# Performance work log

Hardware: AMD Instinct MI355X
Metric: run time of the kernel (lower is better)

The kernel has to match this reference:

```python
import jax, jax.numpy as jnp
import numpy as np

D = 256; NH = 8; NL = 4; NP = 4; DFF = 1024; BS = 8; NQ = 300
DH = D // NH
EPS = 1e-5
SPATIAL = np.array([[100, 150], [50, 75], [25, 38], [13, 19]], dtype=np.int64)  # (H, W) per level
SIZES = (SPATIAL[:, 0] * SPATIAL[:, 1])
S = int(SIZES.sum())  # 19947
LSI = np.concatenate([[0], np.cumsum(SIZES)[:-1]]).astype(np.int64)


def setup_inputs() -> dict:
    key = jax.random.key(0)
    ks = iter(jax.random.split(key, 48))
    def nrm(shape, s=0.02):
        return jax.random.normal(next(ks), shape, jnp.float32) * s
    return {
        "tgt": jax.random.normal(next(ks), (BS, NQ, D), jnp.float32),
        "tgt_query_pos": jax.random.normal(next(ks), (BS, NQ, D), jnp.float32),
        "tgt_reference_points": jax.random.uniform(next(ks), (BS, NQ, NL, 2), jnp.float32),
        "memory": jax.random.normal(next(ks), (BS, S, D), jnp.float32),
        "memory_key_padding_mask": jnp.zeros((BS, S), jnp.bool_),
        "memory_spatial_shapes": jnp.asarray(SPATIAL),
        "memory_level_start_index": jnp.asarray(LSI),
        # self-attention (nn.MultiheadAttention) params
        "in_proj_w": nrm((3 * D, D)), "in_proj_b": jnp.zeros((3 * D,), jnp.float32),
        "out_proj_w": nrm((D, D)), "out_proj_b": jnp.zeros((D,), jnp.float32),
        # layernorms
        "norm1_g": jnp.ones((D,), jnp.float32), "norm1_b": jnp.zeros((D,), jnp.float32),
        "norm2_g": jnp.ones((D,), jnp.float32), "norm2_b": jnp.zeros((D,), jnp.float32),
        "norm3_g": jnp.ones((D,), jnp.float32), "norm3_b": jnp.zeros((D,), jnp.float32),
        # MSDeformAttn params
        "samp_off_w": nrm((NH * NL * NP * 2, D)), "samp_off_b": nrm((NH * NL * NP * 2,), 0.5),
        "attn_wt_w": nrm((NH * NL * NP, D)), "attn_wt_b": jnp.zeros((NH * NL * NP,), jnp.float32),
        "value_w": nrm((D, D)), "value_b": jnp.zeros((D,), jnp.float32),
        "outp_w": nrm((D, D)), "outp_b": jnp.zeros((D,), jnp.float32),
        # FFN params
        "lin1_w": nrm((DFF, D)), "lin1_b": jnp.zeros((DFF,), jnp.float32),
        "lin2_w": nrm((D, DFF)), "lin2_b": jnp.zeros((D,), jnp.float32),
    }


def _ln(x, g, b):
    m = x.mean(-1, keepdims=True)
    v = ((x - m) ** 2).mean(-1, keepdims=True)
    return (x - m) / jnp.sqrt(v + EPS) * g + b


def _self_attn(tgt, pos, in_w, in_b, ow, ob):
    bs, nq, _ = tgt.shape
    qk = tgt + pos
    qw, kw, vw = jnp.split(in_w, 3, axis=0)
    qb, kb, vb = jnp.split(in_b, 3)
    proj = lambda x, w, b: (x @ w.T + b).reshape(bs, nq, NH, DH)
    qh, kh, vh = proj(qk, qw, qb), proj(qk, kw, kb), proj(tgt, vw, vb)
    logits = jnp.einsum('bqhd,bkhd->bhqk', qh, kh) / np.sqrt(DH).astype(np.float32)
    a = jax.nn.softmax(logits, axis=-1)
    o = jnp.einsum('bhqk,bkhd->bqhd', a, vh).reshape(bs, nq, D)
    return o @ ow.T + ob


def _msdeform(query, ref, memory, pad_mask, so_w, so_b, aw_w, aw_b, vw, vb, ow, ob):
    bs, nq, _ = query.shape
    value = memory @ vw.T + vb
    value = jnp.where(pad_mask[..., None], 0.0, value).reshape(bs, S, NH, DH)
    off = (query @ so_w.T + so_b).reshape(bs, nq, NH, NL, NP, 2)
    aw = jax.nn.softmax((query @ aw_w.T + aw_b).reshape(bs, nq, NH, NL * NP), axis=-1)
    aw = aw.reshape(bs, nq, NH, NL, NP)
    # offset normalizer is (W, H) per level
    normalizer = jnp.asarray(SPATIAL[:, ::-1].copy(), jnp.float32)
    locs = ref[:, :, None, :, None, :] + off / normalizer[None, None, None, :, None, :]
    out = jnp.zeros((bs, nq, NH, DH), jnp.float32)
    for l in range(NL):
        Hl, Wl = int(SPATIAL[l, 0]), int(SPATIAL[l, 1])
        s0 = int(LSI[l])
        v = value[:, s0:s0 + Hl * Wl]  # [bs, Hl*Wl, NH, DH]
        # grid_sample(align_corners=False) pixel mapping
        x = locs[:, :, :, l, :, 0] * Wl - 0.5  # [bs, nq, NH, NP]
        y = locs[:, :, :, l, :, 1] * Hl - 0.5
        x0f, y0f = jnp.floor(x), jnp.floor(y)
        tx, ty = x - x0f, y - y0f
        x0, y0 = x0f.astype(jnp.int32), y0f.astype(jnp.int32)
        samp = jnp.zeros(x.shape + (DH,), jnp.float32)
        for dy, dx, w in ((0, 0, (1 - ty) * (1 - tx)), (0, 1, (1 - ty) * tx),
                          (1, 0, ty * (1 - tx)), (1, 1, ty * tx)):
            xi, yi = x0 + dx, y0 + dy
            valid = (xi >= 0) & (xi < Wl) & (yi >= 0) & (yi < Hl)  # zero padding
            idx = jnp.clip(yi, 0, Hl - 1) * Wl + jnp.clip(xi, 0, Wl - 1)
            idx2 = idx.swapaxes(2, 3).reshape(bs, nq * NP, NH)
            g = jnp.take_along_axis(v, idx2[..., None], axis=1)  # [bs, nq*NP, NH, DH]
            g = g.reshape(bs, nq, NP, NH, DH).transpose(0, 1, 3, 2, 4)
            samp = samp + g * (w * valid)[..., None]
        out = out + jnp.einsum('bqhp,bqhpd->bqhd', aw[:, :, :, l], samp)
    return out.reshape(bs, nq, D) @ ow.T + ob


def reference(tgt, tgt_query_pos, tgt_reference_points, memory, memory_key_padding_mask,
              memory_spatial_shapes, memory_level_start_index,
              in_proj_w, in_proj_b, out_proj_w, out_proj_b,
              norm1_g, norm1_b, norm2_g, norm2_b, norm3_g, norm3_b,
              samp_off_w, samp_off_b, attn_wt_w, attn_wt_b,
              value_w, value_b, outp_w, outp_b,
              lin1_w, lin1_b, lin2_w, lin2_b):
    # self-cross ordering (self_cross=True), eval mode (dropout=identity)
    t2 = _self_attn(tgt, tgt_query_pos, in_proj_w, in_proj_b, out_proj_w, out_proj_b)
    tgt = _ln(tgt + t2, norm2_g, norm2_b)
    t2 = _msdeform(tgt + tgt_query_pos, tgt_reference_points, memory, memory_key_padding_mask,
                   samp_off_w, samp_off_b, attn_wt_w, attn_wt_b, value_w, value_b, outp_w, outp_b)
    tgt = _ln(tgt + t2, norm1_g, norm1_b)
    t2 = jax.nn.relu(tgt @ lin1_w.T + lin1_b) @ lin2_w.T + lin2_b
    return _ln(tgt + t2, norm3_g, norm3_b)
```

## Files before the change

kernel.cpp:

```cpp
#include <hip/hip_runtime.h>
#include <hip/hip_bf16.h>

#define D_   256
#define NH_  8
#define NL_  4
#define NP_  4
#define DFF_ 1024
#define BS_  8
#define NQ_  300
#define DH_  32
#define S_TOT 19947
#define EPS_ 1e-5f

typedef __bf16 bf16x8 __attribute__((ext_vector_type(8)));
typedef __bf16 bf16x4 __attribute__((ext_vector_type(4)));
typedef float  f32x4  __attribute__((ext_vector_type(4)));

#define W_INW  0
#define W_OUTW 196608
#define W_SOW  262144
#define W_AWW  327680
#define W_VW   360448
#define W_OPW  425984
#define W_L1W  491520
#define W_L2W  753664
#define W_TOT  1015808

__global__ __launch_bounds__(256) void cast_w_kernel(
    const float* __restrict__ s_inw, const float* __restrict__ s_outw,
    const float* __restrict__ s_sow, const float* __restrict__ s_aww,
    const float* __restrict__ s_vw,  const float* __restrict__ s_opw,
    const float* __restrict__ s_l1w, const float* __restrict__ s_l2w,
    __bf16* __restrict__ dst, __bf16* __restrict__ Wf)
{
    if (blockIdx.x >= 992) {
        const int g = (blockIdx.x - 992) * 256 + threadIdx.x;
        const int l = g & 63;
        const int t = (g >> 6) & 15;
        const int s = g >> 10;
        const int row = t * 16 + (l & 15);
        const int col = s * 32 + (l >> 4) * 8;
        const float* src = s_vw + (size_t)row * 256 + col;
        const float4 v0 = *(const float4*)src;
        const float4 v1 = *(const float4*)(src + 4);
        bf16x8 o;
        o[0] = (__bf16)v0.x; o[1] = (__bf16)v0.y;
        o[2] = (__bf16)v0.z; o[3] = (__bf16)v0.w;
        o[4] = (__bf16)v1.x; o[5] = (__bf16)v1.y;
        o[6] = (__bf16)v1.z; o[7] = (__bf16)v1.w;
        *(bf16x8*)(Wf + (size_t)g * 8) = o;
        return;
    }
    const int i = (blockIdx.x * 256 + threadIdx.x) * 4;
    if (i >= W_TOT) return;
    const float* s; int off;
    if      (i < W_OUTW) { s = s_inw;  off = W_INW;  }
    else if (i < W_SOW)  { s = s_outw; off = W_OUTW; }
    else if (i < W_AWW)  { s = s_sow;  off = W_SOW;  }
    else if (i < W_VW)   { s = s_aww;  off = W_AWW;  }
    else if (i < W_OPW)  { s = s_vw;   off = W_VW;   }
    else if (i < W_L1W)  { s = s_opw;  off = W_OPW;  }
    else if (i < W_L2W)  { s = s_l1w;  off = W_L1W;  }
    else                 { s = s_l2w;  off = W_L2W;  }
    const float4 v = *(const float4*)(s + (i - off));
    bf16x4 o;
    o[0] = (__bf16)v.x; o[1] = (__bf16)v.y;
    o[2] = (__bf16)v.z; o[3] = (__bf16)v.w;
    *(bf16x4*)(dst + i) = o;
}

__global__ __launch_bounds__(512, 4) void gemm_value(
    const float* __restrict__ A, const __bf16* __restrict__ Wf,
    const float* __restrict__ bias, __hip_bfloat16* __restrict__ C, int M)
{
    __shared__ __align__(16) __bf16 As[2][16][264];
    const int tid = threadIdx.x;
    const int wave = tid >> 6, lane = tid & 63;
    const int frow = lane & 15;
    const int k8 = (lane >> 4) * 8;

    bf16x8 bB[2][8];
#pragma unroll
    for (int j = 0; j < 2; ++j) {
        const int t = wave * 2 + j;
#pragma unroll
        for (int s = 0; s < 8; ++s)
            bB[j][s] = *(const bf16x8*)(Wf + ((size_t)(s * 16 + t) * 64 + lane) * 8);
    }
    float bb0 = bias[wave * 32 + frow];
    float bb1 = bias[wave * 32 + 16 + frow];

    const int nt = (M + 15) >> 4;
    const int stride = gridDim.x;
    int tile = blockIdx.x;

    const int srow = tid >> 5;
    const int scol = (tid & 31) * 8;

    {
        int gr = tile * 16 + srow; if (gr >= M) gr = M - 1;
        const float* ap = A + (size_t)gr * 256 + scol;
        const float4 a0 = *(const float4*)ap;
        const float4 a1 = *(const float4*)(ap + 4);
        bf16x8 o;
        o[0] = (__bf16)a0.x; o[1] = (__bf16)a0.y;
        o[2] = (__bf16)a0.z; o[3] = (__bf16)a0.w;
        o[4] = (__bf16)a1.x; o[5] = (__bf16)a1.y;
        o[6] = (__bf16)a1.z; o[7] = (__bf16)a1.w;
        *(bf16x8*)&As[0][srow][scol] = o;
    }
    __syncthreads();

    int buf = 0;
    for (; tile < nt; tile += stride, buf ^= 1) {
        const int nxt = tile + stride;
        const bool have_nxt = nxt < nt;
        float4 p0, p1;
        if (have_nxt) {
            int gr = nxt * 16 + srow; if (gr >= M) gr = M - 1;
            const float* ap = A + (size_t)gr * 256 + scol;
            p0 = *(const float4*)ap;
            p1 = *(const float4*)(ap + 4);
        }

        f32x4 acc0 = (f32x4){0.f, 0.f, 0.f, 0.f};
        f32x4 acc1 = acc0;
#pragma unroll
        for (int s = 0; s < 8; ++s) {
            const bf16x8 aF = *(const bf16x8*)&As[buf][frow][s * 32 + k8];
            acc0 = __builtin_amdgcn_mfma_f32_16x16x32_bf16(aF, bB[0][s], acc0, 0, 0, 0);
            acc1 = __builtin_amdgcn_mfma_f32_16x16x32_bf16(aF, bB[1][s], acc1, 0, 0, 0);
        }

        const int m0 = tile * 16;
        const int row0 = (lane >> 4) * 4;
        const int col0 = wave * 32 + frow;
#pragma unroll
        for (int r = 0; r < 4; ++r) {
            const int gr = m0 + row0 + r;
            if (gr < M) {
                __hip_bfloat16* cp = C + (size_t)gr * 256 + col0;
                cp[0]  = __float2bfloat16(acc0[r] + bb0);
                cp[16] = __float2bfloat16(acc1[r] + bb1);
            }
        }

        if (have_nxt) {
            bf16x8 o;
            o[0] = (__bf16)p0.x; o[1] = (__bf16)p0.y;
            o[2] = (__bf16)p0.z; o[3] = (__bf16)p0.w;
            o[4] = (__bf16)p1.x; o[5] = (__bf16)p1.y;
            o[6] = (__bf16)p1.z; o[7] = (__bf16)p1.w;
            *(bf16x8*)&As[buf ^ 1][srow][scol] = o;
        }
        __syncthreads();
    }
}

__global__ __launch_bounds__(256) void gemm_small(
    const float* __restrict__ A, const float* __restrict__ A2,
    const __bf16* __restrict__ W, const float* __restrict__ bias,
    float* __restrict__ C, int M, int N, int K, int relu,
    const float* __restrict__ bias2, float* __restrict__ C2, int N1)
{
    __shared__ __align__(16) __bf16 As[64][40];
    __shared__ __align__(16) __bf16 Bs[64][40];
    const int tid = threadIdx.x;
    const int wave = tid >> 6, lane = tid & 63;
    const int m0 = blockIdx.x * 64, n0 = blockIdx.y * 64;
    const int frow = lane & 15, fk = (lane >> 4) * 8;

    f32x4 acc[4];
#pragma unroll
    for (int j = 0; j < 4; ++j) acc[j] = (f32x4){0.f, 0.f, 0.f, 0.f};

    const int ar = tid >> 2;
    const int ak = (tid & 3) * 8;
    const bool a_ok = (m0 + ar) < M;
    const bool use_a2 = (A2 != nullptr) && (n0 < N1);

    for (int k0 = 0; k0 < K; k0 += 32) {
        float4 a0 = make_float4(0,0,0,0), a1 = a0;
        if (a_ok) {
            const float* ap = A + (size_t)(m0 + ar) * K + k0 + ak;
            a0 = *(const float4*)ap;
            a1 = *(const float4*)(ap + 4);
            if (use_a2) {
                const float* ap2 = A2 + (size_t)(m0 + ar) * K + k0 + ak;
                const float4 c0 = *(const float4*)ap2;
                const float4 c1 = *(const float4*)(ap2 + 4);
                a0.x += c0.x; a0.y += c0.y; a0.z += c0.z; a0.w += c0.w;
                a1.x += c1.x; a1.y += c1.y; a1.z += c1.z; a1.w += c1.w;
            }
        }
        const bf16x8 b8 = *(const bf16x8*)(W + (size_t)(n0 + ar) * K + k0 + ak);

        __syncthreads();
        bf16x8 w0;
        w0[0] = (__bf16)a0.x; w0[1] = (__bf16)a0.y; w0[2] = (__bf16)a0.z; w0[3] = (__bf16)a0.w;
        w0[4] = (__bf16)a1.x; w0[5] = (__bf16)a1.y; w0[6] = (__bf16)a1.z; w0[7] = (__bf16)a1.w;
        *(bf16x8*)&As[ar][ak] = w0;
        *(bf16x8*)&Bs[ar][ak] = b8;
        __syncthreads();

        const bf16x8 aF = *(const bf16x8*)&As[wave * 16 + frow][fk];
#pragma unroll
        for (int j = 0; j < 4; ++j) {
            const bf16x8 bF = *(const bf16x8*)&Bs[j * 16 + frow][fk];
            acc[j] = __builtin_amdgcn_mfma_f32_16x16x32_bf16(aF, bF, acc[j], 0, 0, 0);
        }
    }

    const int row = m0 + wave * 16 + (lane >> 4) * 4;
#pragma unroll
    for (int j = 0; j < 4; ++j) {
        const int col = n0 + j * 16 + frow;
        float* dst; const float* bsrc; int strideC, ccol;
        if (!C2 || col < N1) { dst = C;  bsrc = bias;  strideC = N1;     ccol = col; }
        else                 { dst = C2; bsrc = bias2; strideC = N - N1; ccol = col - N1; }
        const float bb = bsrc[ccol];
#pragma unroll
        for (int r = 0; r < 4; ++r) {
            if (row + r >= M) continue;
            float val = acc[j][r] + bb;
            if (relu) val = fmaxf(val, 0.f);
            dst[(size_t)(row + r) * strideC + ccol] = val;
        }
    }
}

__global__ __launch_bounds__(256) void attn_fused_kernel(
    const float* __restrict__ qk, const float* __restrict__ v,
    float* __restrict__ attn)
{
    __shared__ __align__(16) __bf16 Vt[32][328];
    __shared__ __align__(16) __bf16 Ps[64][328];
    const int qt = blockIdx.x, bh = blockIdx.y;
    const int b = bh >> 3, h = bh & 7;
    const int tid = threadIdx.x;
    const int wave = tid >> 6, lane = tid & 63;
    const float scale = 0.17677669529663687f;

    {
        const int d = tid & 31;
        for (int kk = tid >> 5; kk < NQ_; kk += 8)
            Vt[d][kk] = (__bf16)v[(size_t)(b * NQ_ + kk) * 256 + h * 32 + d];
        for (int i = tid; i < 32 * 20; i += 256)
            Vt[i & 31][300 + (i >> 5)] = (__bf16)0.f;
        for (int i = tid; i < 64 * 16; i += 256)
            Ps[i & 63][304 + (i >> 6)] = (__bf16)0.f;
    }

    const int m = qt * 64 + wave * 16 + (lane & 15);
    const int k8 = (lane >> 4) * 8;

    bf16x8 aF = {};
    if (m < NQ_) {
        const float* qp = qk + (size_t)(b * NQ_ + m) * 512 + h * 32 + k8;
        const float4 q0 = *(const float4*)qp;
        const float4 q1 = *(const float4*)(qp + 4);
        aF[0] = (__bf16)q0.x; aF[1] = (__bf16)q0.y;
        aF[2] = (__bf16)q0.z; aF[3] = (__bf16)q0.w;
        aF[4] = (__bf16)q1.x; aF[5] = (__bf16)q1.y;
        aF[6] = (__bf16)q1.z; aF[7] = (__bf16)q1.w;
    }

    f32x4 c[19];
#pragma unroll
    for (int t = 0; t < 19; ++t) {
        const int n = t * 16 + (lane & 15);
        bf16x8 bF = {};
        if (n < NQ_) {
            const float* kp = qk + (size_t)(b * NQ_ + n) * 512 + 256 + h * 32 + k8;
            const float4 k0 = *(const float4*)kp;
            const float4 k1 = *(const float4*)(kp + 4);
            bF[0] = (__bf16)k0.x; bF[1] = (__bf16)k0.y;
            bF[2] = (__bf16)k0.z; bF[3] = (__bf16)k0.w;
            bF[4] = (__bf16)k1.x; bF[5] = (__bf16)k1.y;
            bF[6] = (__bf16)k1.z; bF[7] = (__bf16)k1.w;
        }
        f32x4 z = (f32x4){0.f, 0.f, 0.f, 0.f};
        c[t] = __builtin_amdgcn_mfma_f32_16x16x32_bf16(aF, bF, z, 0, 0, 0);
    }

    const int myc = lane & 15;
#pragma unroll
    for (int t = 0; t < 19; ++t) {
        const bool ok = (t * 16 + myc) < NQ_;
#pragma unroll
        for (int r = 0; r < 4; ++r)
            c[t][r] = ok ? c[t][r] * scale : -1e30f;
    }

    float mx[4] = {-1e30f, -1e30f, -1e30f, -1e30f};
#pragma unroll
    for (int t = 0; t < 19; ++t)
#pragma unroll
        for (int r = 0; r < 4; ++r) mx[r] = fmaxf(mx[r], c[t][r]);
#pragma unroll
    for (int off = 8; off; off >>= 1)
#pragma unroll
        for (int r = 0; r < 4; ++r)
            mx[r] = fmaxf(mx[r], __shfl_xor(mx[r], off, 64));

    float sum[4] = {0.f, 0.f, 0.f, 0.f};
#pragma unroll
    for (int t = 0; t < 19; ++t)
#pragma unroll
        for (int r = 0; r < 4; ++r) {
            const float e = __expf(c[t][r] - mx[r]);
            c[t][r] = e;
            sum[r] += e;
        }
#pragma unroll
    for (int off = 8; off; off >>= 1)
#pragma unroll
        for (int r = 0; r < 4; ++r)
            sum[r] += __shfl_xor(sum[r], off, 64);
    float inv[4];
#pragma unroll
    for (int r = 0; r < 4; ++r) inv[r] = 1.f / sum[r];

    const int lrow0 = wave * 16 + (lane >> 4) * 4;
#pragma unroll
    for (int t = 0; t < 19; ++t) {
        const int col = t * 16 + myc;
#pragma unroll
        for (int r = 0; r < 4; ++r)
            Ps[lrow0 + r][col] = (__bf16)(c[t][r] * inv[r]);
    }
    __syncthreads();

    const int lm = wave * 16 + (lane & 15);
    f32x4 acc0 = (f32x4){0.f, 0.f, 0.f, 0.f};
    f32x4 acc1 = acc0;
#pragma unroll
    for (int k0 = 0; k0 < 320; k0 += 32) {
        const bf16x8 pF = *(const bf16x8*)&Ps[lm][k0 + k8];
        const bf16x8 b0 = *(const bf16x8*)&Vt[lane & 15][k0 + k8];
        const bf16x8 b1 = *(const bf16x8*)&Vt[16 + (lane & 15)][k0 + k8];
        acc0 = __builtin_amdgcn_mfma_f32_16x16x32_bf16(pF, b0, acc0, 0, 0, 0);
        acc1 = __builtin_amdgcn_mfma_f32_16x16x32_bf16(pF, b1, acc1, 0, 0, 0);
    }

    const int row0 = qt * 64 + lrow0;
    const int col = lane & 15;
#pragma unroll
    for (int r = 0; r < 4; ++r) {
        if (row0 + r >= NQ_) continue;
        float* op = attn + (size_t)(b * NQ_ + row0 + r) * 256 + h * 32;
        op[col]      = acc0[r];
        op[col + 16] = acc1[r];
    }
}

__global__ __launch_bounds__(256) void ln_kernel(
    const float* __restrict__ x, const float* __restrict__ res,
    const float* __restrict__ g, const float* __restrict__ bt,
    float* __restrict__ out,
    const float* __restrict__ pos, float* __restrict__ out2)
{
    const int row = blockIdx.x;
    const int tid = threadIdx.x;
    const size_t idx = (size_t)row * D_ + tid;
    float v = x[idx] + (res ? res[idx] : 0.f);

    __shared__ float red[4];
    float s = v;
#pragma unroll
    for (int off = 32; off; off >>= 1) s += __shfl_xor(s, off, 64);
    if ((tid & 63) == 0) red[tid >> 6] = s;
    __syncthreads();
    const float mean = (red[0] + red[1] + red[2] + red[3]) * (1.f / D_);
    const float c = v - mean;
    __syncthreads();

    float s2 = c * c;
#pragma unroll
    for (int off = 32; off; off >>= 1) s2 += __shfl_xor(s2, off, 64);
    if ((tid & 63) == 0) red[tid >> 6] = s2;
    __syncthreads();
    const float var = (red[0] + red[1] + red[2] + red[3]) * (1.f / D_);

    const float y = c * rsqrtf(var + EPS_) * g[tid] + bt[tid];
    out[idx] = y;
    if (out2) out2[idx] = y + pos[idx];
}

__global__ __launch_bounds__(256) void msdeform_kernel(
    const float* __restrict__ offs, const float* __restrict__ awl,
    const float* __restrict__ refp, const __hip_bfloat16* __restrict__ value,
    float* __restrict__ samp)
{
    const int rsec = threadIdx.x >> 6;
    const int row = blockIdx.x * 4 + rsec;
    const int b = row / NQ_;
    const int t = threadIdx.x & 63;
    const int h = t >> 3, d4 = t & 7;

    __shared__ float off_s[4][256];
    __shared__ float aw_s[4][128];
    __shared__ float ref_s[4][8];
    off_s[rsec][t]       = offs[(size_t)row * 256 + t];
    off_s[rsec][t + 64]  = offs[(size_t)row * 256 + t + 64];
    off_s[rsec][t + 128] = offs[(size_t)row * 256 + t + 128];
    off_s[rsec][t + 192] = offs[(size_t)row * 256 + t + 192];
    aw_s[rsec][t]        = awl[(size_t)row * 128 + t];
    aw_s[rsec][t + 64]   = awl[(size_t)row * 128 + t + 64];
    if (t < 8) ref_s[rsec][t] = refp[(size_t)row * 8 + t];
    __syncthreads();

    float mx = -1e30f;
#pragma unroll
    for (int i = 0; i < 16; ++i) mx = fmaxf(mx, aw_s[rsec][h * 16 + i]);
    float sum = 0.f;
#pragma unroll
    for (int i = 0; i < 16; ++i) sum += __expf(aw_s[rsec][h * 16 + i] - mx);
    const float winv = 1.f / sum;

    const int Hs[4] = {100, 50, 25, 13};
    const int Wl_[4] = {150, 75, 38, 19};
    const int S0[4] = {0, 15000, 18750, 19700};

    float o0 = 0.f, o1 = 0.f, o2 = 0.f, o3 = 0.f;
    const __hip_bfloat16* vbase = value + ((size_t)b * S_TOT) * D_ + h * 32 + d4 * 4;

#pragma unroll
    for (int l = 0; l < NL_; ++l) {
        const int Hl = Hs[l], Wl = Wl_[l];
        const float rx = ref_s[rsec][l * 2], ry = ref_s[rsec][l * 2 + 1];
        const __hip_bfloat16* vl = vbase + (size_t)S0[l] * D_;
#pragma unroll
        for (int p = 0; p < NP_; ++p) {
            const int oi = ((h * NL_ + l) * NP_ + p) * 2;
            const float lx = rx + off_s[rsec][oi] / (float)Wl;
            const float ly = ry + off_s[rsec][oi + 1] / (float)Hl;
            const float x = lx * Wl - 0.5f;
            const float y = ly * Hl - 0.5f;
            const float x0f = floorf(x), y0f = floorf(y);
            const float tx = x - x0f, ty = y - y0f;
            const int x0 = (int)x0f, y0 = (int)y0f;
            const float aw = __expf(aw_s[rsec][h * 16 + l * 4 + p] - mx) * winv;

            float s0 = 0.f, s1 = 0.f, s2 = 0.f, s3 = 0.f;
#pragma unroll
            for (int cc = 0; cc < 4; ++cc) {
                const int dy = cc >> 1, dx = cc & 1;
                const int xi = x0 + dx, yi = y0 + dy;
                const float w = (dy ? ty : 1.f - ty) * (dx ? tx : 1.f - tx);
                if (xi >= 0 && xi < Wl && yi >= 0 && yi < Hl) {
                    const int idx = yi * Wl + xi;
                    const uint2 u = *(const uint2*)(vl + (size_t)idx * D_);
                    s0 += w * __uint_as_float(u.x << 16);
                    s1 += w * __uint_as_float(u.x & 0xffff0000u);
                    s2 += w * __uint_as_float(u.y << 16);
                    s3 += w * __uint_as_float(u.y & 0xffff0000u);
                }
            }
            o0 += aw * s0;
            o1 += aw * s1;
            o2 += aw * s2;
            o3 += aw * s3;
        }
    }
    float4 ov; ov.x = o0; ov.y = o1; ov.z = o2; ov.w = o3;
    *(float4*)(samp + (size_t)row * 256 + h * 32 + d4 * 4) = ov;
}

extern "C" void kernel_launch(void* const* d_in, const int* in_sizes, int n_in,
                              void* d_out, int out_size, void* d_ws, size_t ws_size,
                              hipStream_t stream)
{
    const float* tgt   = (const float*)d_in[0];
    const float* pos   = (const float*)d_in[1];
    const float* refp  = (const float*)d_in[2];
    const float* memory= (const float*)d_in[3];
    const float* in_w  = (const float*)d_in[7];
    const float* in_b  = (const float*)d_in[8];
    const float* outw  = (const float*)d_in[9];
    const float* outb  = (const float*)d_in[10];
    const float* n1g = (const float*)d_in[11]; const float* n1b = (const float*)d_in[12];
    const float* n2g = (const float*)d_in[13]; const float* n2b = (const float*)d_in[14];
    const float* n3g = (const float*)d_in[15]; const float* n3b = (const float*)d_in[16];
    const float* sow = (const float*)d_in[17]; const float* sob = (const float*)d_in[18];
    const float* aww = (const float*)d_in[19]; const float* awb = (const float*)d_in[20];
    const float* vw  = (const float*)d_in[21]; const float* vb_ = (const float*)d_in[22];
    const float* opw = (const float*)d_in[23]; const float* opb = (const float*)d_in[24];
    const float* l1w = (const float*)d_in[25]; const float* l1b = (const float*)d_in[26];
    const float* l2w = (const float*)d_in[27]; const float* l2b = (const float*)d_in[28];
    float* out = (float*)d_out;

    char* ws = (char*)d_ws;
    size_t o = 0;
    auto alloc = [&](size_t bytes) -> char* {
        char* p = ws + o;
        o += (bytes + 255) & ~(size_t)255;
        return p;
    };

    const int M = BS_ * NQ_;
    __bf16* Wb = (__bf16*)alloc((size_t)W_TOT * 2);
    __bf16* Wf = (__bf16*)alloc((size_t)65536 * 2);
    __hip_bfloat16* value = (__hip_bfloat16*)alloc((size_t)BS_ * S_TOT * D_ * 2);
    float* qk    = (float*)alloc((size_t)M * 512 * 4);
    float* v     = (float*)alloc((size_t)M * 256 * 4);
    float* attn  = (float*)alloc((size_t)M * 256 * 4);
    float* attno = (float*)alloc((size_t)M * 256 * 4);
    float* tgt1  = (float*)alloc((size_t)M * 256 * 4);
    float* query2= (float*)alloc((size_t)M * 256 * 4);
    float* offs  = (float*)alloc((size_t)M * 256 * 4);
    float* awl   = (float*)alloc((size_t)M * 128 * 4);
    float* samp  = (float*)alloc((size_t)M * 256 * 4);
    float* t2m   = (float*)alloc((size_t)M * 256 * 4);
    float* tgt2  = (float*)alloc((size_t)M * 256 * 4);
    float* ffn1  = (float*)alloc((size_t)M * 1024 * 4);
    float* ffn2  = (float*)alloc((size_t)M * 256 * 4);

    const dim3 blk(256);
    const int MB = (M + 63) / 64;

    cast_w_kernel<<<1024, blk, 0, stream>>>(
        in_w, outw, sow, aww, vw, opw, l1w, l2w, Wb, Wf);

    gemm_small<<<dim3(MB, 12), blk, 0, stream>>>(
        tgt, pos, Wb + W_INW, in_b, qk, M, 768, 256, 0, in_b + 512, v, 512);

    attn_fused_kernel<<<dim3(5, 64), blk, 0, stream>>>(qk, v, attn);

    gemm_small<<<dim3(MB, 4), blk, 0, stream>>>(
        attn, nullptr, Wb + W_OUTW, outb, attno, M, 256, 256, 0, nullptr, nullptr, 256);

    ln_kernel<<<M, blk, 0, stream>>>(tgt, attno, n2g, n2b, tgt1, pos, query2);

    gemm_small<<<dim3(MB, 6), blk, 0, stream>>>(
        query2, nullptr, Wb + W_SOW, sob, offs, M, 384, 256, 0, awb, awl, 256);

    gemm_value<<<dim3(512), dim3(512), 0, stream>>>(memory, Wf, vb_, value, BS_ * S_TOT);

    msdeform_kernel<<<M / 4, blk, 0, stream>>>(offs, awl, refp, value, samp);

    gemm_small<<<dim3(MB, 4), blk, 0, stream>>>(
        samp, nullptr, Wb + W_OPW, opb, t2m, M, 256, 256, 0, nullptr, nullptr, 256);

    ln_kernel<<<M, blk, 0, stream>>>(tgt1, t2m, n1g, n1b, tgt2, nullptr, nullptr);

    gemm_small<<<dim3(MB, 16), blk, 0, stream>>>(
        tgt2, nullptr, Wb + W_L1W, l1b, ffn1, M, 1024, 256, 1, nullptr, nullptr, 1024);

    gemm_small<<<dim3(MB, 4), blk, 0, stream>>>(
        ffn1, nullptr, Wb + W_L2W, l2b, ffn2, M, 256, 1024, 0, nullptr, nullptr, 256);

    ln_kernel<<<M, blk, 0, stream>>>(tgt2, ffn2, n3g, n3b, out, nullptr, nullptr);
}
```

Baseline: 435.6 us.

## Store value tensor head-major and fold query+pos add into offset GEMM

The value projection now writes its bf16 output in a [batch][head][S][32] layout, and the deformable sampling kernel indexes it that way. Each head's 32 channels for neighbouring spatial positions are then contiguous, which should improve cache-line use for the bilinear gathers. The tgt+pos sum that the layernorm used to write to a separate buffer is now computed inside the offset/attention-weight GEMM through a new a2_all flag, removing one global write and read. The cost is an integer division per output row in the value GEMM epilogue and writes that are more scattered.

```diff
diff --git a/kernel.cpp b/kernel.cpp
--- a/kernel.cpp
+++ b/kernel.cpp
@@ -134,12 +134,14 @@
 
         const int m0 = tile * 16;
         const int row0 = (lane >> 4) * 4;
-        const int col0 = wave * 32 + frow;
 #pragma unroll
         for (int r = 0; r < 4; ++r) {
             const int gr = m0 + row0 + r;
             if (gr < M) {
-                __hip_bfloat16* cp = C + (size_t)gr * 256 + col0;
+                const int bb_ = gr / S_TOT;
+                const int ss_ = gr - bb_ * S_TOT;
+                __hip_bfloat16* cp =
+                    C + (((size_t)bb_ * 8 + wave) * S_TOT + ss_) * 32 + frow;
                 cp[0]  = __float2bfloat16(acc0[r] + bb0);
                 cp[16] = __float2bfloat16(acc1[r] + bb1);
             }
@@ -161,7 +163,7 @@
     const float* __restrict__ A, const float* __restrict__ A2,
     const __bf16* __restrict__ W, const float* __restrict__ bias,
     float* __restrict__ C, int M, int N, int K, int relu,
-    const float* __restrict__ bias2, float* __restrict__ C2, int N1)
+    const float* __restrict__ bias2, float* __restrict__ C2, int N1, int a2_all)
 {
     __shared__ __align__(16) __bf16 As[64][40];
     __shared__ __align__(16) __bf16 Bs[64][40];
@@ -177,7 +179,7 @@
     const int ar = tid >> 2;
     const int ak = (tid & 3) * 8;
     const bool a_ok = (m0 + ar) < M;
-    const bool use_a2 = (A2 != nullptr) && (n0 < N1);
+    const bool use_a2 = (A2 != nullptr) && (a2_all || n0 < N1);
 
     for (int k0 = 0; k0 < K; k0 += 32) {
         float4 a0 = make_float4(0,0,0,0), a1 = a0;
@@ -423,13 +425,14 @@
     const int S0[4] = {0, 15000, 18750, 19700};
 
     float o0 = 0.f, o1 = 0.f, o2 = 0.f, o3 = 0.f;
-    const __hip_bfloat16* vbase = value + ((size_t)b * S_TOT) * D_ + h * 32 + d4 * 4;
+    const __hip_bfloat16* vbase =
+        value + ((size_t)(b * 8 + h) * S_TOT) * 32 + d4 * 4;
 
 #pragma unroll
     for (int l = 0; l < NL_; ++l) {
         const int Hl = Hs[l], Wl = Wl_[l];
         const float rx = ref_s[rsec][l * 2], ry = ref_s[rsec][l * 2 + 1];
-        const __hip_bfloat16* vl = vbase + (size_t)S0[l] * D_;
+        const __hip_bfloat16* vl = vbase + (size_t)S0[l] * 32;
 #pragma unroll
         for (int p = 0; p < NP_; ++p) {
             const int oi = ((h * NL_ + l) * NP_ + p) * 2;
@@ -450,7 +453,7 @@
                 const float w = (dy ? ty : 1.f - ty) * (dx ? tx : 1.f - tx);
                 if (xi >= 0 && xi < Wl && yi >= 0 && yi < Hl) {
                     const int idx = yi * Wl + xi;
-                    const uint2 u = *(const uint2*)(vl + (size_t)idx * D_);
+                    const uint2 u = *(const uint2*)(vl + (size_t)idx * 32);
                     s0 += w * __uint_as_float(u.x << 16);
                     s1 += w * __uint_as_float(u.x & 0xffff0000u);
                     s2 += w * __uint_as_float(u.y << 16);
@@ -507,7 +510,6 @@
     float* attn  = (float*)alloc((size_t)M * 256 * 4);
     float* attno = (float*)alloc((size_t)M * 256 * 4);
     float* tgt1  = (float*)alloc((size_t)M * 256 * 4);
-    float* query2= (float*)alloc((size_t)M * 256 * 4);
     float* offs  = (float*)alloc((size_t)M * 256 * 4);
     float* awl   = (float*)alloc((size_t)M * 128 * 4);
     float* samp  = (float*)alloc((size_t)M * 256 * 4);
@@ -523,32 +525,32 @@
         in_w, outw, sow, aww, vw, opw, l1w, l2w, Wb, Wf);
 
     gemm_small<<<dim3(MB, 12), blk, 0, stream>>>(
-        tgt, pos, Wb + W_INW, in_b, qk, M, 768, 256, 0, in_b + 512, v, 512);
+        tgt, pos, Wb + W_INW, in_b, qk, M, 768, 256, 0, in_b + 512, v, 512, 0);
 
     attn_fused_kernel<<<dim3(5, 64), blk, 0, stream>>>(qk, v, attn);
 
     gemm_small<<<dim3(MB, 4), blk, 0, stream>>>(
-        attn, nullptr, Wb + W_OUTW, outb, attno, M, 256, 256, 0, nullptr, nullptr, 256);
-
-    ln_kernel<<<M, blk, 0, stream>>>(tgt, attno, n2g, n2b, tgt1, pos, query2);
+        attn, nullptr, Wb + W_OUTW, outb, attno, M, 256, 256, 0, nullptr, nullptr, 256, 0);
+
+    ln_kernel<<<M, blk, 0, stream>>>(tgt, attno, n2g, n2b, tgt1, nullptr, nullptr);
 
     gemm_small<<<dim3(MB, 6), blk, 0, stream>>>(
-        query2, nullptr, Wb + W_SOW, sob, offs, M, 384, 256, 0, awb, awl, 256);
+        tgt1, pos, Wb + W_SOW, sob, offs, M, 384, 256, 0, awb, awl, 256, 1);
 
     gemm_value<<<dim3(512), dim3(512), 0, stream>>>(memory, Wf, vb_, value, BS_ * S_TOT);
 
     msdeform_kernel<<<M / 4, blk, 0, stream>>>(offs, awl, refp, value, samp);
 
     gemm_small<<<dim3(MB, 4), blk, 0, stream>>>(
-        samp, nullptr, Wb + W_OPW, opb, t2m, M, 256, 256, 0, nullptr, nullptr, 256);
+        samp, nullptr, Wb + W_OPW, opb, t2m, M, 256, 256, 0, nullptr, nullptr, 256, 0);
 
     ln_kernel<<<M, blk, 0, stream>>>(tgt1, t2m, n1g, n1b, tgt2, nullptr, nullptr);
 
     gemm_small<<<dim3(MB, 16), blk, 0, stream>>>(
-        tgt2, nullptr, Wb + W_L1W, l1b, ffn1, M, 1024, 256, 1, nullptr, nullptr, 1024);
+        tgt2, nullptr, Wb + W_L1W, l1b, ffn1, M, 1024, 256, 1, nullptr, nullptr, 1024, 0);
 
     gemm_small<<<dim3(MB, 4), blk, 0, stream>>>(
-        ffn1, nullptr, Wb + W_L2W, l2b, ffn2, M, 256, 1024, 0, nullptr, nullptr, 256);
+        ffn1, nullptr, Wb + W_L2W, l2b, ffn2, M, 256, 1024, 0, nullptr, nullptr, 256, 0);
 
     ln_kernel<<<M, blk, 0, stream>>>(tgt2, ffn2, n3g, n3b, out, nullptr, nullptr);
 }
```

Measured after the change: 436.3 us. About the same (+0.1%).
